# Performance work log

Measured on AMD Instinct MI355X. Metric: run time of the kernel, lower is better.

## Reference

```python
import jax, jax.numpy as jnp
import numpy as np

N, T, E, B = 50000, 16, 800000, 2000
EMB, ENC, DEC, OUT_LEN = 32, 64, 128, 25
NEG_SLOPE = 0.1
BN_EPS = 1e-5


def lrelu(x):
    return jnp.where(x >= 0, x, NEG_SLOPE * x)


def gru_encode(xs, Wih, Whh, bih, bhh):
    # xs: [T, N, in] -> final hidden [N, H]   (torch GRU gate order: r, z, n)
    H = Whh.shape[1]

    def step(h, x_t):
        gi = x_t @ Wih.T + bih
        gh = h @ Whh.T + bhh
        i_r, i_z, i_n = jnp.split(gi, 3, axis=-1)
        h_r, h_z, h_n = jnp.split(gh, 3, axis=-1)
        r = jax.nn.sigmoid(i_r + h_r)
        z = jax.nn.sigmoid(i_z + h_z)
        n = jnp.tanh(i_n + r * h_n)
        return (1.0 - z) * n + z * h, None

    h0 = jnp.zeros((xs.shape[1], H), xs.dtype)
    hT, _ = jax.lax.scan(step, h0, xs)
    return hT


def lstm_layer(xs, Wih, Whh, bih, bhh):
    # xs: [T, B, in] -> outputs [T, B, H]   (torch LSTM gate order: i, f, g, o)
    H = Whh.shape[1]

    def step(carry, x_t):
        h, c = carry
        g = x_t @ Wih.T + bih + h @ Whh.T + bhh
        i, f, gg, o = jnp.split(g, 4, axis=-1)
        c = jax.nn.sigmoid(f) * c + jax.nn.sigmoid(i) * jnp.tanh(gg)
        h = jax.nn.sigmoid(o) * jnp.tanh(c)
        return (h, c), h

    z0 = jnp.zeros((xs.shape[1], H), xs.dtype)
    _, hs = jax.lax.scan(step, (z0, z0), xs)
    return hs


def cgconv(x, src, dst, edge_attr, Wf, bf, Ws, bs, gamma, beta, mean, var):
    # PyG CGConv: z = [x_i, x_j, e]; msg = sigmoid(lin_f(z)) * softplus(lin_s(z));
    # out = x + BN(scatter_add(msg, i))
    z = jnp.concatenate([x[dst], x[src], edge_attr], axis=-1)  # [E, 2*ENC+2]
    msg = jax.nn.sigmoid(z @ Wf.T + bf) * jax.nn.softplus(z @ Ws.T + bs)
    agg = jax.ops.segment_sum(msg, dst, num_segments=N)  # [N, ENC]
    agg = (agg - mean) * jax.lax.rsqrt(var + BN_EPS) * gamma + beta
    return x + agg


def setup_inputs() -> dict:
    key = jax.random.key(0)
    ks = jax.random.split(key, 32)

    def rn(k, shape, scale=0.1):
        return jax.random.normal(k, shape, jnp.float32) * scale

    inp = {}
    inp["x"] = jax.random.normal(ks[0], (N, T, 2), jnp.float32)
    inp["edge_index"] = jax.random.randint(ks[1], (2, E), 0, N)
    inp["edge_attr"] = jax.random.normal(ks[2], (E, 2), jnp.float32)
    inp["target_index"] = jnp.sort(jax.random.randint(ks[3], (B,), 0, N))
    inp["W_ip"] = rn(ks[4], (EMB, 2)); inp["b_ip"] = jnp.zeros((EMB,), jnp.float32)
    inp["gru_Wih"] = rn(ks[5], (3 * ENC, EMB)); inp["gru_Whh"] = rn(ks[6], (3 * ENC, ENC))
    inp["gru_bih"] = jnp.zeros((3 * ENC,), jnp.float32); inp["gru_bhh"] = jnp.zeros((3 * ENC,), jnp.float32)
    inp["W_dyn"] = rn(ks[7], (ENC, ENC)); inp["b_dyn"] = jnp.zeros((ENC,), jnp.float32)
    Z = 2 * ENC + 2
    for i, base in ((1, 8), (2, 14)):
        inp[f"cg{i}_Wf"] = rn(ks[base], (ENC, Z)); inp[f"cg{i}_bf"] = jnp.zeros((ENC,), jnp.float32)
        inp[f"cg{i}_Ws"] = rn(ks[base + 1], (ENC, Z)); inp[f"cg{i}_bs"] = jnp.zeros((ENC,), jnp.float32)
        inp[f"cg{i}_gamma"] = jnp.ones((ENC,), jnp.float32); inp[f"cg{i}_beta"] = jnp.zeros((ENC,), jnp.float32)
        inp[f"cg{i}_mean"] = jnp.zeros((ENC,), jnp.float32); inp[f"cg{i}_var"] = jnp.ones((ENC,), jnp.float32)
    inp["W_nbrs"] = rn(ks[20], (ENC, ENC)); inp["b_nbrs"] = jnp.zeros((ENC,), jnp.float32)
    inp["lstm0_Wih"] = rn(ks[21], (4 * DEC, 2 * ENC)); inp["lstm0_Whh"] = rn(ks[22], (4 * DEC, DEC))
    inp["lstm0_bih"] = jnp.zeros((4 * DEC,), jnp.float32); inp["lstm0_bhh"] = jnp.zeros((4 * DEC,), jnp.float32)
    inp["lstm1_Wih"] = rn(ks[23], (4 * DEC, DEC)); inp["lstm1_Whh"] = rn(ks[24], (4 * DEC, DEC))
    inp["lstm1_bih"] = jnp.zeros((4 * DEC,), jnp.float32); inp["lstm1_bhh"] = jnp.zeros((4 * DEC,), jnp.float32)
    inp["W_op"] = rn(ks[25], (2, DEC)); inp["b_op"] = jnp.zeros((2,), jnp.float32)
    return inp


def reference(x, edge_index, edge_attr, target_index, W_ip, b_ip,
              gru_Wih, gru_Whh, gru_bih, gru_bhh, W_dyn, b_dyn,
              cg1_Wf, cg1_bf, cg1_Ws, cg1_bs, cg1_gamma, cg1_beta, cg1_mean, cg1_var,
              cg2_Wf, cg2_bf, cg2_Ws, cg2_bs, cg2_gamma, cg2_beta, cg2_mean, cg2_var,
              W_nbrs, b_nbrs,
              lstm0_Wih, lstm0_Whh, lstm0_bih, lstm0_bhh,
              lstm1_Wih, lstm1_Whh, lstm1_bih, lstm1_bhh, W_op, b_op):
    src, dst = edge_index[0], edge_index[1]
    # --- history encoder (GRU) ---
    h = lrelu(x @ W_ip.T + b_ip)                                  # [N, T, EMB]
    hT = gru_encode(h.transpose(1, 0, 2), gru_Wih, gru_Whh, gru_bih, gru_bhh)  # [N, ENC]
    hist = lrelu(lrelu(hT) @ W_dyn.T + b_dyn)                     # [N, ENC]
    # --- CGConv interaction x2 ---
    f = cgconv(hist, src, dst, edge_attr, cg1_Wf, cg1_bf, cg1_Ws, cg1_bs,
               cg1_gamma, cg1_beta, cg1_mean, cg1_var)
    f = cgconv(f, src, dst, edge_attr, cg2_Wf, cg2_bf, cg2_Ws, cg2_bs,
               cg2_gamma, cg2_beta, cg2_mean, cg2_var)
    tar = lrelu(f[target_index] @ W_nbrs.T + b_nbrs)              # [B, ENC]
    enc = jnp.concatenate([hist[target_index], tar], axis=-1)     # [B, 2*ENC]
    # --- LSTM decoder over repeated encoding ---
    xs = jnp.broadcast_to(enc, (OUT_LEN,) + enc.shape)            # [OUT_LEN, B, 2*ENC]
    hs = lstm_layer(xs, lstm0_Wih, lstm0_Whh, lstm0_bih, lstm0_bhh)
    hs = lstm_layer(hs, lstm1_Wih, lstm1_Whh, lstm1_bih, lstm1_bhh)
    fut = hs.transpose(1, 0, 2) @ W_op.T + b_op                   # [B, OUT_LEN, 2]
    return fut
```

## Files before the change

### kernel.cpp

```cpp
#include <hip/hip_runtime.h>
#include <math.h>

#define NN   50000
#define TT   16
#define EE   800000
#define BB   2000
#define EMBD 32
#define ENC  64
#define DEC  128
#define OUTL 25
#define BN_EPS 1e-5f

typedef short v8s __attribute__((ext_vector_type(8)));
typedef float v4f __attribute__((ext_vector_type(4)));
#define MFMA16(a,b,c) __builtin_amdgcn_mfma_f32_16x16x32_bf16((a),(b),(c),0,0,0)

__device__ __forceinline__ float lrelu(float v){ return v >= 0.f ? v : 0.1f*v; }
__device__ __forceinline__ float fsig(float v){ return __builtin_amdgcn_rcpf(1.f + __expf(-v)); }
__device__ __forceinline__ float ftanh(float v){ return 2.f*__builtin_amdgcn_rcpf(1.f + __expf(-2.f*v)) - 1.f; }
__device__ __forceinline__ float fsoftplus(float v){
    return v > 15.f ? v : __logf(1.f + __expf(v));
}
__device__ __forceinline__ float hsum(float4 a){ return (a.x+a.y)+(a.z+a.w); }

__device__ __forceinline__ unsigned short f2bf(float f){
    unsigned u = __float_as_uint(f);
    u = u + 0x7FFFu + ((u>>16)&1u);
    return (unsigned short)(u>>16);
}
__device__ __forceinline__ float bf2f(unsigned short s){ return __uint_as_float(((unsigned)s)<<16); }

__device__ __forceinline__ void tsplit(float v, unsigned short& hi, unsigned short& lo){
    unsigned u = __float_as_uint(v);
    hi = (unsigned short)(u >> 16);
    float r = v - __uint_as_float(u & 0xFFFF0000u);
    lo = (unsigned short)(__float_as_uint(r) >> 16);
}

__device__ __forceinline__ v8s as_v8s(int4 v){
    union { int4 i; v8s s; } u; u.i = v; return u.s;
}

__device__ __forceinline__ void cvt8(const float* p, v8s& hi, v8s& lo){
    float4 a0 = *(const float4*)p;
    float4 a1 = *(const float4*)(p+4);
    float av[8] = {a0.x,a0.y,a0.z,a0.w,a1.x,a1.y,a1.z,a1.w};
#pragma unroll
    for (int j=0;j<8;j++){
        unsigned short h = f2bf(av[j]);
        hi[j] = (short)h;
        lo[j] = (short)f2bf(av[j] - bf2f(h));
    }
}
__device__ __forceinline__ void lrelu_resplit(v8s hh, v8s hl, v8s& oh, v8s& ol){
#pragma unroll
    for (int j=0;j<8;j++){
        float v = bf2f((unsigned short)hh[j]) + bf2f((unsigned short)hl[j]);
        float a = lrelu(v);
        unsigned short h = f2bf(a);
        oh[j] = (short)h;
        ol[j] = (short)f2bf(a - bf2f(h));
    }
}

__device__ __forceinline__ void pf_item(const float* W, int K, int KB, int i,
                                        unsigned short* out){
    int l = i & 63, fb = i >> 6;
    int kb = fb % KB, nt = fb / KB;
    int n = nt*16 + (l&15);
    int k0 = kb*32 + ((l>>4)*8);
#pragma unroll
    for (int j=0;j<8;j++) out[i*8+j] = f2bf(W[(size_t)n*K + k0 + j]);
}
__device__ __forceinline__ void phl_item(const float* W, int K, int KB, int i,
                                         unsigned short* hi, unsigned short* lo){
    int l = i & 63, fb = i >> 6;
    int kb = fb % KB, nt = fb / KB;
    int n = nt*16 + (l&15);
    int k0 = kb*32 + ((l>>4)*8);
#pragma unroll
    for (int j=0;j<8;j++){
        float v = W[(size_t)n*K + k0 + j];
        unsigned short h = f2bf(v);
        hi[i*8+j] = h;
        lo[i*8+j] = f2bf(v - bf2f(h));
    }
}
__device__ __forceinline__ void pcat_item(const float* Wa, const float* Wb,
                                          int K1, int K, int KB, int i,
                                          unsigned short* out){
    int l = i & 63, fb = i >> 6;
    int kb = fb % KB, nt = fb / KB;
    int n = nt*16 + (l&15);
    int k0 = kb*32 + ((l>>4)*8);
#pragma unroll
    for (int j=0;j<8;j++){
        int k = k0 + j;
        float v = (k < K1) ? Wa[(size_t)n*K1 + k] : Wb[(size_t)n*(K-K1) + (k-K1)];
        out[i*8+j] = f2bf(v);
    }
}
__device__ __forceinline__ void pproj_item(const float* Wf, const float* Ws, int i,
                                           unsigned short* hi, unsigned short* lo){
    int l = i & 63, fb = i >> 6;
    int kb = fb & 1, nt = fb >> 1;
    int n = nt*16 + (l&15);
    int d = n >> 6, c = n & 63;
    const float* W = (d < 2) ? Wf : Ws;
    int k0 = (d&1)*64 + kb*32 + ((l>>4)*8);
#pragma unroll
    for (int j=0;j<8;j++){
        float v = W[c*130 + k0 + j];
        unsigned short h = f2bf(v);
        hi[i*8+j] = h;
        lo[i*8+j] = f2bf(v - bf2f(h));
    }
}

__global__ void pack_all(
    const float* __restrict__ gWih, const float* __restrict__ gWhh,
    const float* __restrict__ Wdyn,
    const float* __restrict__ l0Whh, const float* __restrict__ l1Wih,
    const float* __restrict__ l1Whh, const float* __restrict__ l0Wih,
    const float* __restrict__ c1Wf, const float* __restrict__ c1Ws,
    const float* __restrict__ c2Wf, const float* __restrict__ c2Ws,
    unsigned short* __restrict__ pWih, unsigned short* __restrict__ pWhh,
    unsigned short* __restrict__ pWdyn,
    unsigned short* __restrict__ B0h, unsigned short* __restrict__ B1h,
    unsigned short* __restrict__ P1h, unsigned short* __restrict__ P1l,
    unsigned short* __restrict__ P2h, unsigned short* __restrict__ P2l,
    unsigned short* __restrict__ GIh, unsigned short* __restrict__ GIl,
    int* __restrict__ cnt, int* __restrict__ gtot)
{
    int i = blockIdx.x*256 + threadIdx.x;
    if (i < 768){ pf_item(gWih, 32, 1, i, pWih); return; }   i -= 768;
    if (i < 1536){ pf_item(gWhh, 64, 2, i, pWhh); return; }  i -= 1536;
    if (i < 512){ pf_item(Wdyn, 64, 2, i, pWdyn); return; }  i -= 512;
    if (i < 8192){ pcat_item(l0Whh, l0Whh, 128, 128, 4, i, B0h); return; } i -= 8192;
    if (i < 16384){ pcat_item(l1Wih, l1Whh, 128, 256, 8, i, B1h); return; } i -= 16384;
    if (i < 2048){ pproj_item(c1Wf, c1Ws, i, P1h, P1l); return; } i -= 2048;
    if (i < 2048){ pproj_item(c2Wf, c2Ws, i, P2h, P2l); return; } i -= 2048;
    if (i < 8192){ phl_item(l0Wih, 128, 4, i, GIh, GIl); return; } i -= 8192;
    if (i < NN){ cnt[i] = 0; return; } i -= NN;
    if (i < 1){ gtot[0] = 0; return; }
}
#define PACK_TOTAL (768+1536+512+8192+16384+2048+2048+8192+NN+1)

__global__ __launch_bounds__(256) void encoder_mfma(
    const float* __restrict__ x,
    const float* __restrict__ Wip, const float* __restrict__ bip,
    const unsigned short* __restrict__ pWih,
    const unsigned short* __restrict__ pWhh,
    const float* __restrict__ bih, const float* __restrict__ bhh,
    const unsigned short* __restrict__ pWdyn,
    const float* __restrict__ bdyn,
    float* __restrict__ hist)
{
    __shared__ unsigned short efh[16*512], efl[16*512];
    __shared__ unsigned short hfh[2][1024], hfl[2][1024];
    const int tid = threadIdx.x;
    const int l   = tid & 63;
    const int w   = tid >> 6;
    const int ln  = l & 15, q = l >> 4;
    const int blk = blockIdx.x;
    const int rsw = ((l>>1)&7)<<3;

    for (int i = tid; i < 1024; i += 256){
        hfh[0][i]=0; hfl[0][i]=0; hfh[1][i]=0; hfl[1][i]=0;
    }

    float w0[8], w1[8], bk[8];
#pragma unroll
    for (int j = 0; j < 8; j++){
        int k = q*8 + j;
        w0[j] = Wip[2*k]; w1[j] = Wip[2*k+1]; bk[j] = bip[k];
    }

    const float2* xrow = (const float2*)(x + (size_t)(blk*16 + ln)*32);
#pragma unroll
    for (int tt = 0; tt < 4; tt++){
        int t = w*4 + tt;
        float2 xv = xrow[t];
        v8s eh, el;
#pragma unroll
        for (int j = 0; j < 8; j++){
            float e = lrelu(w0[j]*xv.x + w1[j]*xv.y + bk[j]);
            unsigned short h_, l_;
            tsplit(e, h_, l_);
            eh[j] = (short)h_; el[j] = (short)l_;
        }
        *(v8s*)&efh[t*512 + l*8] = eh;
        *(v8s*)&efl[t*512 + l*8] = el;
    }

    const int c = w*16 + ln;
    const float bR  = bih[c]       + bhh[c];
    const float bZ  = bih[64 + c]  + bhh[64 + c];
    const float bNI = bih[128 + c];
    const float bNH = bhh[128 + c];
    float hprev[4] = {0.f,0.f,0.f,0.f};

    const v8s* FIH = (const v8s*)pWih;
    const v8s* FHH = (const v8s*)pWhh;
    const v8s* FDY = (const v8s*)pWdyn;
    const int wbase = (c>>5)*512 + (16*((c&31)>>3))*8 + (c&7);
    __syncthreads();

    int p = 0;
#pragma unroll 1
    for (int t = 0; t < TT; t++){
        v8s eh  = *(const v8s*)&efh[t*512 + l*8];
        v8s el  = *(const v8s*)&efl[t*512 + l*8];
        v8s h0h = *(const v8s*)&hfh[p][(l*8) ^ rsw];
        v8s h0l = *(const v8s*)&hfl[p][(l*8) ^ rsw];
        v8s h1h = *(const v8s*)&hfh[p][512 + ((l*8) ^ rsw)];
        v8s h1l = *(const v8s*)&hfl[p][512 + ((l*8) ^ rsw)];

        v4f aR = {bR,bR,bR,bR};
        v4f aZ = {bZ,bZ,bZ,bZ};
        v4f aNI= {bNI,bNI,bNI,bNI};
        v4f aNH= {bNH,bNH,bNH,bNH};
        v8s b;
        b = FIH[(w   )*64 + l];    aR = MFMA16(eh,b,aR);  aR = MFMA16(el,b,aR);
        b = FHH[(w*2+0)*64+l];     aR = MFMA16(h0h,b,aR); aR = MFMA16(h0l,b,aR);
        b = FHH[(w*2+1)*64+l];     aR = MFMA16(h1h,b,aR); aR = MFMA16(h1l,b,aR);
        b = FIH[(4+w )*64 + l];    aZ = MFMA16(eh,b,aZ);  aZ = MFMA16(el,b,aZ);
        b = FHH[((4+w)*2+0)*64+l]; aZ = MFMA16(h0h,b,aZ); aZ = MFMA16(h0l,b,aZ);
        b = FHH[((4+w)*2+1)*64+l]; aZ = MFMA16(h1h,b,aZ); aZ = MFMA16(h1l,b,aZ);
        b = FIH[(8+w )*64 + l];    aNI= MFMA16(eh,b,aNI); aNI= MFMA16(el,b,aNI);
        b = FHH[((8+w)*2+0)*64+l]; aNH= MFMA16(h0h,b,aNH);aNH= MFMA16(h0l,b,aNH);
        b = FHH[((8+w)*2+1)*64+l]; aNH= MFMA16(h1h,b,aNH);aNH= MFMA16(h1l,b,aNH);

#pragma unroll
        for (int i = 0; i < 4; i++){
            float r_ = fsig(aR[i]);
            float z_ = fsig(aZ[i]);
            float nn_ = ftanh(aNI[i] + r_*aNH[i]);
            float hn = nn_ + z_*(hprev[i] - nn_);
            hprev[i] = hn;
            int row = q*4 + i;
            int off = (wbase + row*8) ^ ((((row)>>1)&7)<<3);
            unsigned short hh_, hl_;
            tsplit(hn, hh_, hl_);
            hfh[1-p][off] = hh_;
            hfl[1-p][off] = hl_;
        }
        __syncthreads();
        p ^= 1;
    }
    {
        v8s a0h,a0l,a1h,a1l;
        lrelu_resplit(*(const v8s*)&hfh[p][(l*8) ^ rsw],
                      *(const v8s*)&hfl[p][(l*8) ^ rsw],       a0h, a0l);
        lrelu_resplit(*(const v8s*)&hfh[p][512 + ((l*8) ^ rsw)],
                      *(const v8s*)&hfl[p][512 + ((l*8) ^ rsw)], a1h, a1l);
        const int nt = w;
        float bb = bdyn[nt*16 + ln];
        v4f acc = {bb,bb,bb,bb};
        v8s b;
        b = FDY[(nt*2+0)*64 + l]; acc = MFMA16(a0h,b,acc); acc = MFMA16(a0l,b,acc);
        b = FDY[(nt*2+1)*64 + l]; acc = MFMA16(a1h,b,acc); acc = MFMA16(a1l,b,acc);
#pragma unroll
        for (int i = 0; i < 4; i++){
            hist[(size_t)(blk*16 + q*4 + i)*64 + nt*16 + ln] = lrelu(acc[i]);
        }
    }
}

__global__ __launch_bounds__(256) void proj_mfma(
    const float* __restrict__ xin,
    const unsigned short* __restrict__ Bh, const unsigned short* __restrict__ Bl,
    float* __restrict__ Af, float* __restrict__ Bf,
    float* __restrict__ As, float* __restrict__ Bs)
{
    __shared__ float sx[64*68];
    const int tid = threadIdx.x;
    const int l = tid & 63;
    const int w = tid >> 6;
    const int ln = l & 15, q = l >> 4;
    const int n0 = blockIdx.x*64;

    for (int i=tid;i<64*16;i+=256){
        int nn = i>>4, f4 = i&15;
        float4 v = {0.f,0.f,0.f,0.f};
        if (n0+nn < NN) v = ((const float4*)(xin + (size_t)(n0+nn)*64))[f4];
        *(float4*)&sx[nn*68 + f4*4] = v;
    }
    __syncthreads();

    v8s ah0,al0,ah1,al1;
    cvt8(&sx[(w*16+ln)*68 +      q*8], ah0, al0);
    cvt8(&sx[(w*16+ln)*68 + 32 + q*8], ah1, al1);

    const v8s* FH = (const v8s*)Bh;
    const v8s* FL = (const v8s*)Bl;
#pragma unroll 1
    for (int nt=0; nt<16; nt++){
        v8s bh0 = FH[(nt*2+0)*64 + l], bl0 = FL[(nt*2+0)*64 + l];
        v8s bh1 = FH[(nt*2+1)*64 + l], bl1 = FL[(nt*2+1)*64 + l];
        v4f acc = {0.f,0.f,0.f,0.f};
        acc = MFMA16(ah0,bh0,acc); acc = MFMA16(al0,bh0,acc); acc = MFMA16(ah0,bl0,acc);
        acc = MFMA16(ah1,bh1,acc); acc = MFMA16(al1,bh1,acc); acc = MFMA16(ah1,bl1,acc);
        int d = nt >> 2, col = (nt&3)*16 + ln;
        float* op = (d==0) ? Af : (d==1) ? Bf : (d==2) ? As : Bs;
#pragma unroll
        for (int i=0;i<4;i++){
            int node = n0 + w*16 + q*4 + i;
            if (node < NN) op[(size_t)node*64 + col] = acc[i];
        }
    }
}

__global__ void count_kernel(const int* __restrict__ ei, int* __restrict__ cnt){
    int e = blockIdx.x*256 + threadIdx.x;
    if (e < EE) atomicAdd(&cnt[ei[EE+e]], 1);
}

__global__ void alloc_kernel(const int* __restrict__ cnt, int* __restrict__ gtot,
                             int* __restrict__ off, int* __restrict__ cur){
    int n = blockIdx.x*256 + threadIdx.x;
    if (n >= NN) return;
    int c = cnt[n];
    int s = atomicAdd(gtot, c);
    off[n] = s;
    cur[n] = s;
}

__global__ void scatter_kernel(const int* __restrict__ ei, const float* __restrict__ ea,
                               int* __restrict__ cur, int4* __restrict__ recS){
    int e = blockIdx.x*256 + threadIdx.x;
    if (e >= EE) return;
    int d = ei[EE+e];
    int p = atomicAdd(&cur[d], 1);
    int4 r;
    r.x = ei[e];
    r.y = __float_as_int(ea[2*(size_t)e]);
    r.z = __float_as_int(ea[2*(size_t)e+1]);
    r.w = 0;
    recS[p] = r;
}

__global__ __launch_bounds__(256) void cg_agg(
    const float* __restrict__ xin,
    const int4* __restrict__ recS,
    const int* __restrict__ off, const int* __restrict__ cnt,
    const float* __restrict__ Wf, const float* __restrict__ bf,
    const float* __restrict__ Ws, const float* __restrict__ bs,
    const float* __restrict__ Af, const float* __restrict__ Bf,
    const float* __restrict__ As, const float* __restrict__ Bs,
    const float* __restrict__ gamma, const float* __restrict__ beta,
    const float* __restrict__ mean, const float* __restrict__ var,
    float* __restrict__ outp)
{
    const int tid = threadIdx.x;
    const int c = tid & 63, wid = tid >> 6;
    const int n = blockIdx.x*4 + wid;
    if (n >= NN) return;

    const float wf0 = Wf[c*130+128], wf1 = Wf[c*130+129], bfc = bf[c];
    const float ws0 = Ws[c*130+128], ws1 = Ws[c*130+129], bsc = bs[c];
    const float afd = Af[(size_t)n*64+c] + bfc, asd = As[(size_t)n*64+c] + bsc;
    const float* Bfc = Bf + c;
    const float* Bsc = Bs + c;

    float acc = 0.f;
    int i = off[n];
    const int i1 = i + cnt[n];
#pragma unroll 1
    for (; i+1 < i1; i += 2){
        int4 r0 = recS[i], r1 = recS[i+1];
        float e00 = __int_as_float(r0.y), e01 = __int_as_float(r0.z);
        float e10 = __int_as_float(r1.y), e11 = __int_as_float(r1.z);
        float bf0v = Bfc[(size_t)r0.x*64], bs0v = Bsc[(size_t)r0.x*64];
        float bf1v = Bfc[(size_t)r1.x*64], bs1v = Bsc[(size_t)r1.x*64];
        float gf0 = afd + bf0v + wf0*e00 + wf1*e01;
        float gs0 = asd + bs0v + ws0*e00 + ws1*e01;
        float gf1 = afd + bf1v + wf0*e10 + wf1*e11;
        float gs1 = asd + bs1v + ws0*e10 + ws1*e11;
        acc += fsig(gf0)*fsoftplus(gs0);
        acc += fsig(gf1)*fsoftplus(gs1);
    }
    if (i < i1){
        int4 r0 = recS[i];
        float e00 = __int_as_float(r0.y), e01 = __int_as_float(r0.z);
        float gf = afd + Bfc[(size_t)r0.x*64] + wf0*e00 + wf1*e01;
        float gs = asd + Bsc[(size_t)r0.x*64] + ws0*e00 + ws1*e01;
        acc += fsig(gf)*fsoftplus(gs);
    }
    float bn = (acc - mean[c])*rsqrtf(var[c]+BN_EPS)*gamma[c] + beta[c];
    outp[(size_t)n*64+c] = xin[(size_t)n*64+c] + bn;
}

__global__ __launch_bounds__(256) void target_kernel(
    const float* __restrict__ hist, const float* __restrict__ f2,
    const int* __restrict__ tgt,
    const float* __restrict__ Wn, const float* __restrict__ bn_,
    float* __restrict__ enc)
{
    const int tid=threadIdx.x;
    const int c = tid&63, q = tid>>6;
    const int b = blockIdx.x*4 + q;
    if (b>=BB) return;
    const int n = tgt[b];
    float a = bn_[c];
#pragma unroll
    for (int k=0;k<ENC;k++) a += Wn[c*64+k]*f2[(size_t)n*64+k];
    enc[(size_t)b*128 + 64 + c] = lrelu(a);
    enc[(size_t)b*128 + c]      = hist[(size_t)n*64+c];
}

__global__ __launch_bounds__(512) void gi0_mfma(
    const float* __restrict__ enc,
    const unsigned short* __restrict__ GIh, const unsigned short* __restrict__ GIl,
    const float* __restrict__ bih0, const float* __restrict__ bhh0,
    float* __restrict__ gi0)
{
    __shared__ float senc[16*132];
    const int tid = threadIdx.x;
    const int l = tid & 63;
    const int w = tid >> 6;
    const int ln = l & 15, q = l >> 4;
    const int b0 = blockIdx.x*16;

    for (int i=tid;i<16*32;i+=512){
        int row = i>>5, f4 = i&31;
        *(float4*)&senc[row*132 + f4*4] = ((const float4*)(enc + (size_t)(b0+row)*128))[f4];
    }
    __syncthreads();

    v8s ah[4], al[4];
#pragma unroll
    for (int kb=0;kb<4;kb++) cvt8(&senc[ln*132 + kb*32 + q*8], ah[kb], al[kb]);

    const v8s* FH = (const v8s*)GIh;
    const v8s* FL = (const v8s*)GIl;
#pragma unroll
    for (int u=0;u<4;u++){
        int nt = w*4 + u;
        int col = nt*16 + ln;
        float bb = bih0[col] + bhh0[col];
        v4f acc = {bb,bb,bb,bb};
#pragma unroll
        for (int kb=0;kb<4;kb++){
            v8s bh = FH[(nt*4+kb)*64 + l];
            v8s bl = FL[(nt*4+kb)*64 + l];
            acc = MFMA16(ah[kb],bh,acc); acc = MFMA16(al[kb],bh,acc); acc = MFMA16(ah[kb],bl,acc);
        }
#pragma unroll
        for (int i=0;i<4;i++)
            gi0[(size_t)(b0 + q*4 + i)*512 + col] = acc[i];
    }
}

#define LMB 16
__global__ __launch_bounds__(512)
__attribute__((amdgpu_waves_per_eu(2,2)))
void lstm_mfma(
    const float* __restrict__ gi0,
    const unsigned short* __restrict__ B0h,
    const unsigned short* __restrict__ B1h,
    const float* __restrict__ bih1, const float* __restrict__ bhh1,
    float* __restrict__ h1buf)
{
    __shared__ int4 sW0[32*4*64];
    __shared__ unsigned short h0hi[2][4*512], h0lo[2][4*512];
    __shared__ unsigned short h1hi[2][4*512], h1lo[2][4*512];
    const int tid = threadIdx.x;
    const int l = tid & 63;
    const int w = tid >> 6;
    const int c = l & 15;
    const int q = l >> 4;
    const int j = w*16 + c;
    const int b0 = blockIdx.x*LMB;
    const int lsw = ((l>>1)&7)<<3;

    {
        const int4* F0 = (const int4*)B0h;
        for (int i=tid;i<32*4*64;i+=512) sW0[i] = F0[i];
    }
    for (int i=tid;i<4*512;i+=512){
        h0hi[0][i]=0; h0lo[0][i]=0; h0hi[1][i]=0; h0lo[1][i]=0;
        h1hi[0][i]=0; h1lo[0][i]=0; h1hi[1][i]=0; h1lo[1][i]=0;
    }

    int4 W1r[32];
    {
        const int4* F1 = (const int4*)B1h;
#pragma unroll
        for (int g=0;g<4;g++)
#pragma unroll
            for (int kb=0;kb<8;kb++) W1r[g*8+kb] = F1[((g*8+w)*8 + kb)*64 + l];
#pragma unroll
        for (int i=0;i<32;i++)
            asm volatile("" : "+v"(W1r[i].x), "+v"(W1r[i].y), "+v"(W1r[i].z), "+v"(W1r[i].w));
    }

    float rgi[4][4];
#pragma unroll
    for (int g=0;g<4;g++)
#pragma unroll
        for (int i=0;i<4;i++)
            rgi[g][i] = gi0[(size_t)(b0 + q*4 + i)*512 + g*128 + j];

    float b1[4];
#pragma unroll
    for (int g=0;g<4;g++) b1[g] = bih1[g*128+j] + bhh1[g*128+j];
    float c0[4] = {0,0,0,0}, c1[4] = {0,0,0,0};
    const int kbw = j>>5, qw = (j>>3)&3, jw = j&7;
    __syncthreads();

    int p = 0;
#pragma unroll 1
    for (int t=0;t<OUTL;t++){
        v4f aH[4], aL[4];
#pragma unroll
        for (int g=0;g<4;g++){
            v4f t4 = {rgi[g][0], rgi[g][1], rgi[g][2], rgi[g][3]};
            aH[g] = t4;
            v4f z = {0.f,0.f,0.f,0.f};
            aL[g] = z;
        }
#pragma unroll
        for (int kb=0;kb<4;kb++){
            v8s ah = *(const v8s*)&h0hi[p][kb*512 + ((l*8) ^ lsw)];
            v8s al = *(const v8s*)&h0lo[p][kb*512 + ((l*8) ^ lsw)];
#pragma unroll
            for (int g=0;g<4;g++){
                v8s bfr = as_v8s(sW0[((g*8+w)*4 + kb)*64 + l]);
                aH[g] = MFMA16(ah, bfr, aH[g]);
                aL[g] = MFMA16(al, bfr, aL[g]);
            }
        }
#pragma unroll
        for (int i=0;i<4;i++){
            float gi_ = aH[0][i]+aL[0][i], gf_ = aH[1][i]+aL[1][i];
            float gg_ = aH[2][i]+aL[2][i], go_ = aH[3][i]+aL[3][i];
            c0[i] = fsig(gf_)*c0[i] + fsig(gi_)*ftanh(gg_);
            float hn = fsig(go_)*ftanh(c0[i]);
            int row = q*4 + i;
            int off = (kbw*512 + (qw*16 + row)*8 + jw) ^ (((row>>1)&7)<<3);
            unsigned short h = f2bf(hn);
            h0hi[1-p][off] = h;
            h0lo[1-p][off] = f2bf(hn - bf2f(h));
        }
        __syncthreads();

        v4f bH[4], bL[4];
#pragma unroll
        for (int g=0;g<4;g++){
            v4f t4={b1[g],b1[g],b1[g],b1[g]}; bH[g]=t4;
            v4f z={0.f,0.f,0.f,0.f}; bL[g]=z;
        }
#pragma unroll
        for (int kb=0;kb<8;kb++){
            const unsigned short* hb = (kb<4) ? h0hi[1-p] : h1hi[p];
            const unsigned short* lb = (kb<4) ? h0lo[1-p] : h1lo[p];
            int kk = kb & 3;
            v8s ah = *(const v8s*)&hb[kk*512 + ((l*8) ^ lsw)];
            v8s al = *(const v8s*)&lb[kk*512 + ((l*8) ^ lsw)];
#pragma unroll
            for (int g=0;g<4;g++){
                bH[g] = MFMA16(ah, as_v8s(W1r[g*8+kb]), bH[g]);
                bL[g] = MFMA16(al, as_v8s(W1r[g*8+kb]), bL[g]);
            }
        }
        float h1new[4];
#pragma unroll
        for (int i=0;i<4;i++){
            float gi_ = bH[0][i]+bL[0][i], gf_ = bH[1][i]+bL[1][i];
            float gg_ = bH[2][i]+bL[2][i], go_ = bH[3][i]+bL[3][i];
            c1[i] = fsig(gf_)*c1[i] + fsig(gi_)*ftanh(gg_);
            h1new[i] = fsig(go_)*ftanh(c1[i]);
            int row = q*4 + i;
            int off = (kbw*512 + (qw*16 + row)*8 + jw) ^ (((row>>1)&7)<<3);
            unsigned short h = f2bf(h1new[i]);
            h1hi[1-p][off] = h;
            h1lo[1-p][off] = f2bf(h1new[i] - bf2f(h));
        }

#pragma unroll
        for (int i=0;i<4;i++){
            h1buf[((size_t)(b0 + q*4 + i)*OUTL + t)*DEC + j] = h1new[i];
        }
        p ^= 1;
    }
}

__global__ __launch_bounds__(256) void out_proj(
    const float* __restrict__ h1buf,
    const float* __restrict__ Wop, const float* __restrict__ bop,
    float* __restrict__ outp)
{
    int idx = blockIdx.x*256 + threadIdx.x;
    if (idx >= BB*OUTL) return;
    const float4* hp = (const float4*)(h1buf + (size_t)idx*DEC);
    const float4* w0 = (const float4*)Wop;
    const float4* w1 = (const float4*)(Wop + DEC);
    float a0 = 0.f, a1 = 0.f;
#pragma unroll
    for (int k=0;k<32;k++){
        float4 h = hp[k], x0 = w0[k], x1 = w1[k];
        a0 += h.x*x0.x + h.y*x0.y + h.z*x0.z + h.w*x0.w;
        a1 += h.x*x1.x + h.y*x1.y + h.z*x1.z + h.w*x1.w;
    }
    outp[(size_t)idx*2    ] = a0 + bop[0];
    outp[(size_t)idx*2 + 1] = a1 + bop[1];
}

extern "C" void kernel_launch(void* const* d_in, const int* in_sizes, int n_in,
                              void* d_out, int out_size, void* d_ws, size_t ws_size,
                              hipStream_t stream)
{
    const float* x    = (const float*)d_in[0];
    const int*   ei   = (const int*)d_in[1];
    const float* ea   = (const float*)d_in[2];
    const int*   tgt  = (const int*)d_in[3];
    const float* Wip  = (const float*)d_in[4];
    const float* bip  = (const float*)d_in[5];
    const float* gWih = (const float*)d_in[6];
    const float* gWhh = (const float*)d_in[7];
    const float* gbih = (const float*)d_in[8];
    const float* gbhh = (const float*)d_in[9];
    const float* Wdyn = (const float*)d_in[10];
    const float* bdyn = (const float*)d_in[11];
    const float* c1Wf=(const float*)d_in[12]; const float* c1bf=(const float*)d_in[13];
    const float* c1Ws=(const float*)d_in[14]; const float* c1bs=(const float*)d_in[15];
    const float* c1g =(const float*)d_in[16]; const float* c1b =(const float*)d_in[17];
    const float* c1m =(const float*)d_in[18]; const float* c1v =(const float*)d_in[19];
    const float* c2Wf=(const float*)d_in[20]; const float* c2bf=(const float*)d_in[21];
    const float* c2Ws=(const float*)d_in[22]; const float* c2bs=(const float*)d_in[23];
    const float* c2g =(const float*)d_in[24]; const float* c2b =(const float*)d_in[25];
    const float* c2m =(const float*)d_in[26]; const float* c2v =(const float*)d_in[27];
    const float* Wn  =(const float*)d_in[28]; const float* bn_ =(const float*)d_in[29];
    const float* l0Wih=(const float*)d_in[30]; const float* l0Whh=(const float*)d_in[31];
    const float* l0bih=(const float*)d_in[32]; const float* l0bhh=(const float*)d_in[33];
    const float* l1Wih=(const float*)d_in[34]; const float* l1Whh=(const float*)d_in[35];
    const float* l1bih=(const float*)d_in[36]; const float* l1bhh=(const float*)d_in[37];
    const float* Wop =(const float*)d_in[38]; const float* bop=(const float*)d_in[39];

    float* ws = (float*)d_ws;
    size_t o = 0;
    float* hist = ws + o; o += (size_t)NN*ENC;
    float* f1   = ws + o; o += (size_t)NN*ENC;
    float* f2   = ws + o; o += (size_t)NN*ENC;
    float* Af   = ws + o; o += (size_t)NN*ENC;
    float* Bf   = ws + o; o += (size_t)NN*ENC;
    float* As   = ws + o; o += (size_t)NN*ENC;
    float* Bs   = ws + o; o += (size_t)NN*ENC;
    float* enc  = ws + o; o += (size_t)BB*2*ENC;
    float* gi0  = ws + o; o += (size_t)BB*4*DEC;
    unsigned short* pWih  = (unsigned short*)(ws + o); o += (size_t)12*64*8/2;
    unsigned short* pWhh  = (unsigned short*)(ws + o); o += (size_t)24*64*8/2;
    unsigned short* pWdyn = (unsigned short*)(ws + o); o += (size_t)8*64*8/2;
    unsigned short* B0h = (unsigned short*)(ws + o); o += (size_t)32*4*64*8/2;
    unsigned short* B1h = (unsigned short*)(ws + o); o += (size_t)32*8*64*8/2;
    unsigned short* P1h = (unsigned short*)(ws + o); o += (size_t)2048*8/2;
    unsigned short* P1l = (unsigned short*)(ws + o); o += (size_t)2048*8/2;
    unsigned short* P2h = (unsigned short*)(ws + o); o += (size_t)2048*8/2;
    unsigned short* P2l = (unsigned short*)(ws + o); o += (size_t)2048*8/2;
    unsigned short* GIh = (unsigned short*)(ws + o); o += (size_t)8192*8/2;
    unsigned short* GIl = (unsigned short*)(ws + o); o += (size_t)8192*8/2;
    int* cnt    = (int*)(ws + o); o += NN;
    int* offv   = (int*)(ws + o); o += NN+1;
    int* curv   = (int*)(ws + o); o += NN;
    int* gtot   = (int*)(ws + o); o += 1;
    o = (o + 3) & ~(size_t)3;
    int4* recS  = (int4*)(ws + o); o += (size_t)4*EE;

    float* h1buf = Af;

    pack_all<<<(PACK_TOTAL+255)/256, 256, 0, stream>>>(
        gWih, gWhh, Wdyn, l0Whh, l1Wih, l1Whh, l0Wih,
        c1Wf, c1Ws, c2Wf, c2Ws,
        pWih, pWhh, pWdyn, B0h, B1h, P1h, P1l, P2h, P2l, GIh, GIl, cnt, gtot);

    count_kernel<<<(EE+255)/256, 256, 0, stream>>>(ei, cnt);
    alloc_kernel<<<(NN+255)/256, 256, 0, stream>>>(cnt, gtot, offv, curv);
    scatter_kernel<<<(EE+255)/256, 256, 0, stream>>>(ei, ea, curv, recS);

    encoder_mfma<<<NN/16, 256, 0, stream>>>(x, Wip, bip, pWih, pWhh, gbih, gbhh, pWdyn, bdyn, hist);

    proj_mfma<<<(NN+63)/64, 256, 0, stream>>>(hist, P1h, P1l, Af,Bf,As,Bs);
    cg_agg<<<(NN+3)/4, 256, 0, stream>>>(hist, recS, offv, cnt,
                                         c1Wf,c1bf,c1Ws,c1bs, Af,Bf,As,Bs,
                                         c1g,c1b,c1m,c1v, f1);

    proj_mfma<<<(NN+63)/64, 256, 0, stream>>>(f1, P2h, P2l, Af,Bf,As,Bs);
    cg_agg<<<(NN+3)/4, 256, 0, stream>>>(f1, recS, offv, cnt,
                                         c2Wf,c2bf,c2Ws,c2bs, Af,Bf,As,Bs,
                                         c2g,c2b,c2m,c2v, f2);

    target_kernel<<<(BB+3)/4, 256, 0, stream>>>(hist, f2, tgt, Wn, bn_, enc);

    gi0_mfma<<<BB/16, 512, 0, stream>>>(enc, GIh, GIl, l0bih, l0bhh, gi0);

    lstm_mfma<<<BB/LMB, 512, 0, stream>>>(gi0, B0h, B1h,
                                          l1bih, l1bhh, h1buf);

    out_proj<<<(BB*OUTL+255)/256, 256, 0, stream>>>(h1buf, Wop, bop, (float*)d_out);
}
```

Measured before the change: 588.9 us.

## Stream GRU input embeddings in 4-step chunks to shrink encoder LDS and raise occupancy

The encoder used to precompute embeddings for all 16 timesteps into LDS (two 16KB arrays). It now computes them in chunks of four timesteps, with each thread handling one embedding channel for two rows. This cuts the embedding LDS to a quarter, and the launch-bounds hint now asks for 8 blocks per CU. The aim is higher occupancy to hide the serial recurrence latency, at the cost of an extra barrier per chunk and global loads interleaved into the time loop.

New measurement: 764.8 us. 29.9% more time.

```diff
diff --git a/kernel.cpp b/kernel.cpp
--- a/kernel.cpp
+++ b/kernel.cpp
@@ -146,7 +146,7 @@
 }
 #define PACK_TOTAL (768+1536+512+8192+16384+2048+2048+8192+NN+1)
 
-__global__ __launch_bounds__(256) void encoder_mfma(
+__global__ __launch_bounds__(256, 8) void encoder_mfma(
     const float* __restrict__ x,
     const float* __restrict__ Wip, const float* __restrict__ bip,
     const unsigned short* __restrict__ pWih,
@@ -156,7 +156,7 @@
     const float* __restrict__ bdyn,
     float* __restrict__ hist)
 {
-    __shared__ unsigned short efh[16*512], efl[16*512];
+    __shared__ unsigned short efh[4*512], efl[4*512];
     __shared__ unsigned short hfh[2][1024], hfl[2][1024];
     const int tid = threadIdx.x;
     const int l   = tid & 63;
@@ -169,29 +169,12 @@
         hfh[0][i]=0; hfl[0][i]=0; hfh[1][i]=0; hfl[1][i]=0;
     }
 
-    float w0[8], w1[8], bk[8];
-#pragma unroll
-    for (int j = 0; j < 8; j++){
-        int k = q*8 + j;
-        w0[j] = Wip[2*k]; w1[j] = Wip[2*k+1]; bk[j] = bip[k];
-    }
-
-    const float2* xrow = (const float2*)(x + (size_t)(blk*16 + ln)*32);
-#pragma unroll
-    for (int tt = 0; tt < 4; tt++){
-        int t = w*4 + tt;
-        float2 xv = xrow[t];
-        v8s eh, el;
-#pragma unroll
-        for (int j = 0; j < 8; j++){
-            float e = lrelu(w0[j]*xv.x + w1[j]*xv.y + bk[j]);
-            unsigned short h_, l_;
-            tsplit(e, h_, l_);
-            eh[j] = (short)h_; el[j] = (short)l_;
-        }
-        *(v8s*)&efh[t*512 + l*8] = eh;
-        *(v8s*)&efl[t*512 + l*8] = el;
-    }
+    const int k0 = tid & 31;
+    const int mb = tid >> 5;
+    const float ew0 = Wip[2*k0], ew1 = Wip[2*k0+1], ebk = bip[k0];
+    const int ebase = (k0>>3)*128 + (k0&7);
+    const float2* xr0 = (const float2*)(x + (size_t)(blk*16 + 2*mb    )*32);
+    const float2* xr1 = (const float2*)(x + (size_t)(blk*16 + 2*mb + 1)*32);
 
     const int c = w*16 + ln;
     const float bR  = bih[c]       + bhh[c];
@@ -208,45 +191,63 @@
 
     int p = 0;
 #pragma unroll 1
-    for (int t = 0; t < TT; t++){
-        v8s eh  = *(const v8s*)&efh[t*512 + l*8];
-        v8s el  = *(const v8s*)&efl[t*512 + l*8];
-        v8s h0h = *(const v8s*)&hfh[p][(l*8) ^ rsw];
-        v8s h0l = *(const v8s*)&hfl[p][(l*8) ^ rsw];
-        v8s h1h = *(const v8s*)&hfh[p][512 + ((l*8) ^ rsw)];
-        v8s h1l = *(const v8s*)&hfl[p][512 + ((l*8) ^ rsw)];
-
-        v4f aR = {bR,bR,bR,bR};
-        v4f aZ = {bZ,bZ,bZ,bZ};
-        v4f aNI= {bNI,bNI,bNI,bNI};
-        v4f aNH= {bNH,bNH,bNH,bNH};
-        v8s b;
-        b = FIH[(w   )*64 + l];    aR = MFMA16(eh,b,aR);  aR = MFMA16(el,b,aR);
-        b = FHH[(w*2+0)*64+l];     aR = MFMA16(h0h,b,aR); aR = MFMA16(h0l,b,aR);
-        b = FHH[(w*2+1)*64+l];     aR = MFMA16(h1h,b,aR); aR = MFMA16(h1l,b,aR);
-        b = FIH[(4+w )*64 + l];    aZ = MFMA16(eh,b,aZ);  aZ = MFMA16(el,b,aZ);
-        b = FHH[((4+w)*2+0)*64+l]; aZ = MFMA16(h0h,b,aZ); aZ = MFMA16(h0l,b,aZ);
-        b = FHH[((4+w)*2+1)*64+l]; aZ = MFMA16(h1h,b,aZ); aZ = MFMA16(h1l,b,aZ);
-        b = FIH[(8+w )*64 + l];    aNI= MFMA16(eh,b,aNI); aNI= MFMA16(el,b,aNI);
-        b = FHH[((8+w)*2+0)*64+l]; aNH= MFMA16(h0h,b,aNH);aNH= MFMA16(h0l,b,aNH);
-        b = FHH[((8+w)*2+1)*64+l]; aNH= MFMA16(h1h,b,aNH);aNH= MFMA16(h1l,b,aNH);
-
-#pragma unroll
-        for (int i = 0; i < 4; i++){
-            float r_ = fsig(aR[i]);
-            float z_ = fsig(aZ[i]);
-            float nn_ = ftanh(aNI[i] + r_*aNH[i]);
-            float hn = nn_ + z_*(hprev[i] - nn_);
-            hprev[i] = hn;
-            int row = q*4 + i;
-            int off = (wbase + row*8) ^ ((((row)>>1)&7)<<3);
-            unsigned short hh_, hl_;
-            tsplit(hn, hh_, hl_);
-            hfh[1-p][off] = hh_;
-            hfl[1-p][off] = hl_;
+    for (int tb = 0; tb < 4; tb++){
+#pragma unroll
+        for (int ts = 0; ts < 4; ts++){
+            int t = tb*4 + ts;
+            float2 xv0 = xr0[t], xv1 = xr1[t];
+            float e0 = lrelu(ew0*xv0.x + ew1*xv0.y + ebk);
+            float e1 = lrelu(ew0*xv1.x + ew1*xv1.y + ebk);
+            unsigned short h_, l_;
+            tsplit(e0, h_, l_);
+            efh[ts*512 + ebase + (2*mb  )*8] = h_;
+            efl[ts*512 + ebase + (2*mb  )*8] = l_;
+            tsplit(e1, h_, l_);
+            efh[ts*512 + ebase + (2*mb+1)*8] = h_;
+            efl[ts*512 + ebase + (2*mb+1)*8] = l_;
         }
         __syncthreads();
-        p ^= 1;
+#pragma unroll 1
+        for (int ts = 0; ts < 4; ts++){
+            v8s eh  = *(const v8s*)&efh[ts*512 + l*8];
+            v8s el  = *(const v8s*)&efl[ts*512 + l*8];
+            v8s h0h = *(const v8s*)&hfh[p][(l*8) ^ rsw];
+            v8s h0l = *(const v8s*)&hfl[p][(l*8) ^ rsw];
+            v8s h1h = *(const v8s*)&hfh[p][512 + ((l*8) ^ rsw)];
+            v8s h1l = *(const v8s*)&hfl[p][512 + ((l*8) ^ rsw)];
+
+            v4f aR = {bR,bR,bR,bR};
+            v4f aZ = {bZ,bZ,bZ,bZ};
+            v4f aNI= {bNI,bNI,bNI,bNI};
+            v4f aNH= {bNH,bNH,bNH,bNH};
+            v8s b;
+            b = FIH[(w   )*64 + l];    aR = MFMA16(eh,b,aR);  aR = MFMA16(el,b,aR);
+            b = FHH[(w*2+0)*64+l];     aR = MFMA16(h0h,b,aR); aR = MFMA16(h0l,b,aR);
+            b = FHH[(w*2+1)*64+l];     aR = MFMA16(h1h,b,aR); aR = MFMA16(h1l,b,aR);
+            b = FIH[(4+w )*64 + l];    aZ = MFMA16(eh,b,aZ);  aZ = MFMA16(el,b,aZ);
+            b = FHH[((4+w)*2+0)*64+l]; aZ = MFMA16(h0h,b,aZ); aZ = MFMA16(h0l,b,aZ);
+            b = FHH[((4+w)*2+1)*64+l]; aZ = MFMA16(h1h,b,aZ); aZ = MFMA16(h1l,b,aZ);
+            b = FIH[(8+w )*64 + l];    aNI= MFMA16(eh,b,aNI); aNI= MFMA16(el,b,aNI);
+            b = FHH[((8+w)*2+0)*64+l]; aNH= MFMA16(h0h,b,aNH);aNH= MFMA16(h0l,b,aNH);
+            b = FHH[((8+w)*2+1)*64+l]; aNH= MFMA16(h1h,b,aNH);aNH= MFMA16(h1l,b,aNH);
+
+#pragma unroll
+            for (int i = 0; i < 4; i++){
+                float r_ = fsig(aR[i]);
+                float z_ = fsig(aZ[i]);
+                float nn_ = ftanh(aNI[i] + r_*aNH[i]);
+                float hn = nn_ + z_*(hprev[i] - nn_);
+                hprev[i] = hn;
+                int row = q*4 + i;
+                int off = (wbase + row*8) ^ ((((row)>>1)&7)<<3);
+                unsigned short hh_, hl_;
+                tsplit(hn, hh_, hl_);
+                hfh[1-p][off] = hh_;
+                hfl[1-p][off] = hl_;
+            }
+            __syncthreads();
+            p ^= 1;
+        }
     }
     {
         v8s a0h,a0l,a1h,a1l;
```
